# Optimization experiments

Hardware: AMD Instinct MI355X
Metric: run time of the kernel (lower is better)

The kernel has to match this reference:

```python
import jax, jax.numpy as jnp
import numpy as np

DT = 0.01  # time-grid spacing


def _get_A(ts, omega_sq, gamma_0, gamma_amp, omega_d):
    # ts: [...]; returns [..., 2, 2] system matrix A(t)
    gamma = gamma_0 * (1.0 + gamma_amp * jnp.sin(omega_d * ts))
    z = jnp.zeros_like(ts)
    o = jnp.ones_like(ts)
    row0 = jnp.stack([z, o], axis=-1)
    row1 = jnp.stack([-omega_sq * o, -gamma], axis=-1)
    return jnp.stack([row0, row1], axis=-2)


def _expm2x2(M):
    # Closed-form matrix exponential for batched 2x2 matrices [..., 2, 2].
    a, b = M[..., 0, 0], M[..., 0, 1]
    c, d = M[..., 1, 0], M[..., 1, 1]
    m = 0.5 * (a + d)                 # trace/2
    det = a * d - b * c
    delta = m * m - det               # discriminant
    s = jnp.sqrt(jnp.abs(delta))
    pos = delta >= 0
    small = s < 1e-6
    s_safe = jnp.where(small, 1.0, s)
    cosl = jnp.where(pos, jnp.cosh(s), jnp.cos(s))
    sinch = jnp.where(small, 1.0,
                      jnp.where(pos, jnp.sinh(s_safe), jnp.sin(s_safe)) / s_safe)
    I = jnp.eye(2, dtype=M.dtype)
    em = jnp.exp(m)[..., None, None]
    return em * (cosl[..., None, None] * I
                 + sinch[..., None, None] * (M - m[..., None, None] * I))


def setup_inputs() -> dict:
    key = jax.random.key(0)
    k1, = jax.random.split(key, 1)
    T, B = 8192, 4096
    t = jnp.arange(T, dtype=jnp.float32) * DT
    x0 = jax.random.normal(k1, (2, B), dtype=jnp.float32)
    return {
        "t": t,
        "x0": x0,
        "omega_sq": jnp.float32(1.2),
        "gamma_0": jnp.float32(0.35),
        "gamma_amp": jnp.float32(0.15),
        "omega_d": jnp.float32(1.1),
        "use_commutator": 1,
    }


def reference(t, x0, omega_sq, gamma_0, gamma_amp, omega_d, use_commutator):
    t0 = t[:-1]                      # [T-1]
    dt = t[1:] - t[:-1]              # [T-1]
    A0 = _get_A(t0, omega_sq, gamma_0, gamma_amp, omega_d)
    A_mid = _get_A(t0 + dt / 2, omega_sq, gamma_0, gamma_amp, omega_d)
    A1 = _get_A(t0 + dt, omega_sq, gamma_0, gamma_amp, omega_d)
    Omega = A_mid * dt[:, None, None]               # Magnus-1 term
    if use_commutator:
        comm = A0 @ A1 - A1 @ A0                    # [T-1, 2, 2]
        Omega = Omega + (dt ** 2 / 12.0)[:, None, None] * comm
    E = _expm2x2(Omega)                             # [T-1, 2, 2] propagators

    def step(x, Ei):
        xn = Ei @ x                                 # [2, B]
        return xn, xn

    _, ys = jax.lax.scan(step, x0, E)
    return jnp.concatenate([x0[None], ys], axis=0)  # [T, 2, B]
```

## Files before the change

kernel.cpp:

```cpp
#include <hip/hip_runtime.h>


struct M2 { float a, b, c, d; };

__device__ __forceinline__ M2 mmul(const M2& X, const M2& Y) {
    M2 r;
    r.a = X.a * Y.a + X.b * Y.c;
    r.b = X.a * Y.b + X.b * Y.d;
    r.c = X.c * Y.a + X.d * Y.c;
    r.d = X.c * Y.b + X.d * Y.d;
    return r;
}

__global__ void e_kernel(const float* __restrict__ t,
                         const float* __restrict__ p_w2,
                         const float* __restrict__ p_g0,
                         const float* __restrict__ p_ga,
                         const float* __restrict__ p_wd,
                         const int* __restrict__ p_uc,
                         float4* __restrict__ E, int T) {
    int n = blockIdx.x * blockDim.x + threadIdx.x;
    if (n >= T - 1) return;
    float w2 = *p_w2, g0 = *p_g0, ga = *p_ga, wd = *p_wd;
    int uc = *p_uc;

    float t0 = t[n], t1 = t[n + 1];
    float dt = t1 - t0;
    float tm = t0 + dt * 0.5f;

    float gam0 = g0 * (1.0f + ga * sinf(wd * t0));
    float gamm = g0 * (1.0f + ga * sinf(wd * tm));
    float gam1 = g0 * (1.0f + ga * sinf(wd * t1));

    float Oa = 0.0f;
    float Ob = dt;
    float Oc = -w2 * dt;
    float Od = -gamm * dt;
    if (uc) {
        float k = dt * dt * (1.0f / 12.0f);
        float del = gam0 - gam1;
        Ob += k * del;
        Oc += k * (w2 * del);
    }

    float m   = 0.5f * (Oa + Od);
    float det = Oa * Od - Ob * Oc;
    float delta = m * m - det;
    float s = sqrtf(fabsf(delta));
    bool pos = delta >= 0.0f;
    bool small_ = s < 1e-6f;
    float s_safe = small_ ? 1.0f : s;
    float cosl = pos ? coshf(s) : cosf(s);
    float sn   = pos ? sinhf(s_safe) : sinf(s_safe);
    float sinch = small_ ? 1.0f : sn / s_safe;
    float em = expf(m);

    float4 Ev;
    Ev.x = em * (cosl + sinch * (Oa - m));
    Ev.y = em * (sinch * Ob);
    Ev.z = em * (sinch * Oc);
    Ev.w = em * (cosl + sinch * (Od - m));
    E[n] = Ev;
}

__global__ __launch_bounds__(1024) void scan_kernel(const float4* __restrict__ E,
                                                    float4* __restrict__ P, int T) {
    __shared__ float4 lds[1024];
    const int j = threadIdx.x;
    const int base = j * 8;

    M2 S[8];
    #pragma unroll
    for (int mi = 0; mi < 8; ++mi) {
        int k = base + mi;
        M2 Mk;
        if (k < T - 1) {
            float4 e = E[k];
            Mk.a = e.x; Mk.b = e.y; Mk.c = e.z; Mk.d = e.w;
        } else {
            Mk.a = 1.0f; Mk.b = 0.0f; Mk.c = 0.0f; Mk.d = 1.0f;
        }
        S[mi] = (mi == 0) ? Mk : mmul(Mk, S[mi - 1]);
    }

    M2 acc = S[7];
    lds[j] = make_float4(acc.a, acc.b, acc.c, acc.d);
    for (int d = 1; d < 1024; d <<= 1) {
        __syncthreads();
        M2 prev;
        bool act = (j >= d);
        if (act) {
            float4 p = lds[j - d];
            prev.a = p.x; prev.b = p.y; prev.c = p.z; prev.d = p.w;
        }
        __syncthreads();
        if (act) {
            acc = mmul(acc, prev);
            lds[j] = make_float4(acc.a, acc.b, acc.c, acc.d);
        }
    }
    __syncthreads();

    M2 Bm;
    if (j == 0) { Bm.a = 1.0f; Bm.b = 0.0f; Bm.c = 0.0f; Bm.d = 1.0f; }
    else {
        float4 p = lds[j - 1];
        Bm.a = p.x; Bm.b = p.y; Bm.c = p.z; Bm.d = p.w;
    }

    if (j == 0) P[0] = make_float4(1.0f, 0.0f, 0.0f, 1.0f);
    #pragma unroll
    for (int mi = 0; mi < 8; ++mi) {
        int g = base + mi + 1;
        if (g < T) {
            M2 r = mmul(S[mi], Bm);
            P[g] = make_float4(r.a, r.b, r.c, r.d);
        }
    }
}

__global__ __launch_bounds__(256) void out_kernel(const float4* __restrict__ P,
                                                  const float* __restrict__ x0,
                                                  float* __restrict__ out, int B) {
    const int n = blockIdx.x;
    const float4 p = P[n];
    const float4* xr0 = (const float4*)x0;
    const float4* xr1 = xr0 + (B >> 2);
    float4* o = (float4*)(out + (size_t)n * (size_t)(2 * B));
    const int q = B >> 2;

    for (int g = threadIdx.x; g < q; g += blockDim.x) {
        float4 u = xr0[g];
        float4 v = xr1[g];
        float4 r0, r1;
        r0.x = p.x * u.x + p.y * v.x;
        r0.y = p.x * u.y + p.y * v.y;
        r0.z = p.x * u.z + p.y * v.z;
        r0.w = p.x * u.w + p.y * v.w;
        r1.x = p.z * u.x + p.w * v.x;
        r1.y = p.z * u.y + p.w * v.y;
        r1.z = p.z * u.z + p.w * v.z;
        r1.w = p.z * u.w + p.w * v.w;
        o[g]     = r0;
        o[q + g] = r1;
    }
}

extern "C" void kernel_launch(void* const* d_in, const int* in_sizes, int n_in,
                              void* d_out, int out_size, void* d_ws, size_t ws_size,
                              hipStream_t stream) {
    const float* t   = (const float*)d_in[0];
    const float* x0  = (const float*)d_in[1];
    const float* w2  = (const float*)d_in[2];
    const float* g0  = (const float*)d_in[3];
    const float* ga  = (const float*)d_in[4];
    const float* wd  = (const float*)d_in[5];
    const int*   uc  = (const int*)d_in[6];

    const int T = in_sizes[0];
    const int B = in_sizes[1] / 2;

    float4* E = (float4*)d_ws;
    float4* P = E + T;

    float* out = (float*)d_out;

    int nE = T - 1;
    e_kernel<<<(nE + 255) / 256, 256, 0, stream>>>(t, w2, g0, ga, wd, uc, E, T);
    scan_kernel<<<1, 1024, 0, stream>>>(E, P, T);
    out_kernel<<<T, 256, 0, stream>>>(P, x0, out, B);
}
```

Before: 283.6 us.

## Fuse propagator computation into scan and retile output kernel over time rows

Removes the separate e_kernel by computing each 2x2 propagator inside the single-block scan kernel, so one launch and one global round trip of E are gone. The output kernel is restructured so each thread loads its x0 column once and writes 16 consecutive time rows, instead of one block per time row reloading x0. The fused scan puts the transcendental work for 8 steps per thread onto a single 1024-thread block, which serialises work that used to be spread across the GPU.

```diff
diff --git a/kernel.cpp b/kernel.cpp
--- a/kernel.cpp
+++ b/kernel.cpp
@@ -12,71 +12,61 @@
     return r;
 }
 
-__global__ void e_kernel(const float* __restrict__ t,
-                         const float* __restrict__ p_w2,
-                         const float* __restrict__ p_g0,
-                         const float* __restrict__ p_ga,
-                         const float* __restrict__ p_wd,
-                         const int* __restrict__ p_uc,
-                         float4* __restrict__ E, int T) {
-    int n = blockIdx.x * blockDim.x + threadIdx.x;
-    if (n >= T - 1) return;
-    float w2 = *p_w2, g0 = *p_g0, ga = *p_ga, wd = *p_wd;
-    int uc = *p_uc;
-
-    float t0 = t[n], t1 = t[n + 1];
-    float dt = t1 - t0;
-    float tm = t0 + dt * 0.5f;
-
-    float gam0 = g0 * (1.0f + ga * sinf(wd * t0));
-    float gamm = g0 * (1.0f + ga * sinf(wd * tm));
-    float gam1 = g0 * (1.0f + ga * sinf(wd * t1));
-
-    float Oa = 0.0f;
-    float Ob = dt;
-    float Oc = -w2 * dt;
-    float Od = -gamm * dt;
-    if (uc) {
-        float k = dt * dt * (1.0f / 12.0f);
-        float del = gam0 - gam1;
-        Ob += k * del;
-        Oc += k * (w2 * del);
-    }
-
-    float m   = 0.5f * (Oa + Od);
-    float det = Oa * Od - Ob * Oc;
-    float delta = m * m - det;
-    float s = sqrtf(fabsf(delta));
-    bool pos = delta >= 0.0f;
-    bool small_ = s < 1e-6f;
-    float s_safe = small_ ? 1.0f : s;
-    float cosl = pos ? coshf(s) : cosf(s);
-    float sn   = pos ? sinhf(s_safe) : sinf(s_safe);
-    float sinch = small_ ? 1.0f : sn / s_safe;
-    float em = expf(m);
-
-    float4 Ev;
-    Ev.x = em * (cosl + sinch * (Oa - m));
-    Ev.y = em * (sinch * Ob);
-    Ev.z = em * (sinch * Oc);
-    Ev.w = em * (cosl + sinch * (Od - m));
-    E[n] = Ev;
-}
-
-__global__ __launch_bounds__(1024) void scan_kernel(const float4* __restrict__ E,
+__global__ __launch_bounds__(1024) void scan_kernel(const float* __restrict__ t,
+                                                    const float* __restrict__ p_w2,
+                                                    const float* __restrict__ p_g0,
+                                                    const float* __restrict__ p_ga,
+                                                    const float* __restrict__ p_wd,
+                                                    const int* __restrict__ p_uc,
                                                     float4* __restrict__ P, int T) {
     __shared__ float4 lds[1024];
     const int j = threadIdx.x;
     const int base = j * 8;
 
+    const float w2 = *p_w2, g0 = *p_g0, ga = *p_ga, wd = *p_wd;
+    const int uc = *p_uc;
+
     M2 S[8];
     #pragma unroll
     for (int mi = 0; mi < 8; ++mi) {
-        int k = base + mi;
+        const int k = base + mi;
         M2 Mk;
         if (k < T - 1) {
-            float4 e = E[k];
-            Mk.a = e.x; Mk.b = e.y; Mk.c = e.z; Mk.d = e.w;
+            float t0 = t[k], t1 = t[k + 1];
+            float dt = t1 - t0;
+            float tm = t0 + dt * 0.5f;
+
+            float gam0 = g0 * (1.0f + ga * sinf(wd * t0));
+            float gamm = g0 * (1.0f + ga * sinf(wd * tm));
+            float gam1 = g0 * (1.0f + ga * sinf(wd * t1));
+
+            float Oa = 0.0f;
+            float Ob = dt;
+            float Oc = -w2 * dt;
+            float Od = -gamm * dt;
+            if (uc) {
+                float kk = dt * dt * (1.0f / 12.0f);
+                float del = gam0 - gam1;
+                Ob += kk * del;
+                Oc += kk * (w2 * del);
+            }
+
+            float m   = 0.5f * (Oa + Od);
+            float det = Oa * Od - Ob * Oc;
+            float delta = m * m - det;
+            float s = sqrtf(fabsf(delta));
+            bool pos = delta >= 0.0f;
+            bool small_ = s < 1e-6f;
+            float s_safe = small_ ? 1.0f : s;
+            float cosl = pos ? coshf(s) : cosf(s);
+            float sn   = pos ? sinhf(s_safe) : sinf(s_safe);
+            float sinch = small_ ? 1.0f : sn / s_safe;
+            float em = expf(m);
+
+            Mk.a = em * (cosl + sinch * (Oa - m));
+            Mk.b = em * (sinch * Ob);
+            Mk.c = em * (sinch * Oc);
+            Mk.d = em * (cosl + sinch * (Od - m));
         } else {
             Mk.a = 1.0f; Mk.b = 0.0f; Mk.c = 0.0f; Mk.d = 1.0f;
         }
@@ -119,19 +109,28 @@
     }
 }
 
+#define NPB 16
 __global__ __launch_bounds__(256) void out_kernel(const float4* __restrict__ P,
                                                   const float* __restrict__ x0,
-                                                  float* __restrict__ out, int B) {
-    const int n = blockIdx.x;
-    const float4 p = P[n];
+                                                  float* __restrict__ out,
+                                                  int B, int T) {
+    const int q = B >> 2;
+    const int g = blockIdx.x * 256 + threadIdx.x;
+    if (g >= q) return;
+
     const float4* xr0 = (const float4*)x0;
-    const float4* xr1 = xr0 + (B >> 2);
-    float4* o = (float4*)(out + (size_t)n * (size_t)(2 * B));
-    const int q = B >> 2;
+    const float4 u = xr0[g];
+    const float4 v = xr0[q + g];
 
-    for (int g = threadIdx.x; g < q; g += blockDim.x) {
-        float4 u = xr0[g];
-        float4 v = xr1[g];
+    const int n0 = blockIdx.y * NPB;
+    const size_t rowStride = (size_t)(2 * B);
+
+    #pragma unroll
+    for (int i = 0; i < NPB; ++i) {
+        const int n = n0 + i;
+        if (n >= T) break;
+        const float4 p = P[n];
+
         float4 r0, r1;
         r0.x = p.x * u.x + p.y * v.x;
         r0.y = p.x * u.y + p.y * v.y;
@@ -141,6 +140,8 @@
         r1.y = p.z * u.y + p.w * v.y;
         r1.z = p.z * u.z + p.w * v.z;
         r1.w = p.z * u.w + p.w * v.w;
+
+        float4* o = (float4*)(out + (size_t)n * rowStride);
         o[g]     = r0;
         o[q + g] = r1;
     }
@@ -160,13 +161,12 @@
     const int T = in_sizes[0];
     const int B = in_sizes[1] / 2;
 
-    float4* E = (float4*)d_ws;
-    float4* P = E + T;
-
+    float4* P = (float4*)d_ws;
     float* out = (float*)d_out;
 
-    int nE = T - 1;
-    e_kernel<<<(nE + 255) / 256, 256, 0, stream>>>(t, w2, g0, ga, wd, uc, E, T);
-    scan_kernel<<<1, 1024, 0, stream>>>(E, P, T);
-    out_kernel<<<T, 256, 0, stream>>>(P, x0, out, B);
+    scan_kernel<<<1, 1024, 0, stream>>>(t, w2, g0, ga, wd, uc, P, T);
+
+    const int q = B >> 2;
+    dim3 grid((q + 255) / 256, (T + NPB - 1) / NPB);
+    out_kernel<<<grid, 256, 0, stream>>>(P, x0, out, B, T);
 }
```

Measured after the change: 285.7 us. No clear change (+0.7%).
